# Kernel tuning notes

Hardware: AMD Instinct MI355X
Metric: run time of the kernel (lower is better)

## Reference

```python
import jax, jax.numpy as jnp
import numpy as np

N_NODES = 50000
N_EDGES = 800000
F_IN, H, C1, C2 = 256, 128, 4, 3


def gcn_conv(x, W, b, src, dst, n_nodes):
    # PyG GCNConv: add self-loops, symmetric normalization D^-1/2 A D^-1/2,
    # linear transform, scatter-add aggregation at dst, then bias.
    loop = jnp.arange(n_nodes, dtype=src.dtype)
    s = jnp.concatenate([src, loop])
    d = jnp.concatenate([dst, loop])
    deg = jax.ops.segment_sum(jnp.ones_like(d, dtype=x.dtype), d, num_segments=n_nodes)
    dinv = jnp.where(deg > 0, jax.lax.rsqrt(deg), 0.0)
    norm = dinv[s] * dinv[d]                      # [E+N]
    h = x @ W                                     # [N, out]
    msg = h[s] * norm[:, None]                    # gather + scale
    out = jax.ops.segment_sum(msg, d, num_segments=n_nodes)  # scatter-add
    return out + b


def setup_inputs() -> dict:
    key = jax.random.key(0)
    ks = jax.random.split(key, 10)
    x = jax.random.normal(ks[0], (N_NODES, F_IN), dtype=jnp.float32)
    edge_index = jax.random.randint(ks[1], (2, N_EDGES), 0, N_NODES, dtype=jnp.int32)
    def lin(k, fan_in, fan_out):
        bound = 1.0 / np.sqrt(fan_in)
        kw, kb = jax.random.split(k)
        W = jax.random.uniform(kw, (fan_in, fan_out), jnp.float32, -bound, bound)
        b = jax.random.uniform(kb, (fan_out,), jnp.float32, -bound, bound)
        return W, b
    W1, b1 = lin(ks[2], F_IN, H)
    W2, b2 = lin(ks[3], H, H)
    Wh1, bh1 = lin(ks[4], H, C1)
    Wh2, bh2 = lin(ks[5], H, C2)
    return {"x": x, "edge_index": edge_index, "W1": W1, "b1": b1,
            "W2": W2, "b2": b2, "Wh1": Wh1, "bh1": bh1, "Wh2": Wh2, "bh2": bh2}


def reference(x, edge_index, W1, b1, W2, b2, Wh1, bh1, Wh2, bh2):
    # Eval-mode forward (dropout p=0.5 is identity at inference; l2_classifier=False).
    src, dst = edge_index[0], edge_index[1]
    h = gcn_conv(x, W1, b1, src, dst, N_NODES)
    h = jax.nn.relu(h)
    h = gcn_conv(h, W2, b2, src, dst, N_NODES)
    out1 = h @ Wh1 + bh1
    out2 = h @ Wh2 + bh2
    return (out1, out2, h)
```

## Files before the change

kernel.cpp:

```cpp
#include <hip/hip_runtime.h>

#define NN 50000
#define NE 800000
#define FIN 256
#define HD 128
#define CAP 96

typedef unsigned int uint;
typedef unsigned short ushort;
typedef __attribute__((ext_vector_type(8))) short short8v;
typedef __attribute__((ext_vector_type(4))) float f32x4;

__device__ inline ushort f2bf(float f) {
    uint u = __float_as_uint(f);
    u += 0x7fffu + ((u >> 16) & 1u);
    return (ushort)(u >> 16);
}
__device__ inline void unpack2(uint u, float& a, float& b) {
    a = __uint_as_float(u << 16);
    b = __uint_as_float(u & 0xffff0000u);
}


__global__ void build_buckets(const int* __restrict__ ei, int* __restrict__ cnt,
                              int* __restrict__ bucket) {
    int e = blockIdx.x * 256 + threadIdx.x;
    if (e >= NE) return;
    int s = ei[e];
    int d = ei[NE + e];
    int pos = atomicAdd(&cnt[d], 1);
    if (pos < CAP) bucket[d * CAP + pos] = s;
}

__global__ void compute_dinv(const int* __restrict__ cnt, float* __restrict__ dinv) {
    int v = blockIdx.x * 256 + threadIdx.x;
    if (v < NN) dinv[v] = rsqrtf((float)cnt[v] + 1.0f);
}


template<int K>
__global__ void prep_wt(const float* __restrict__ W, ushort* __restrict__ Wt) {
    int idx = blockIdx.x * 256 + threadIdx.x;
    if (idx >= K * 128) return;
    int k = idx >> 7, col = idx & 127;
    Wt[col * K + k] = f2bf(W[idx]);
}


template<int K>
__global__ __launch_bounds__(256) void gemm_mfma(const float* __restrict__ A,
                                                 const ushort* __restrict__ Wt,
                                                 const float* __restrict__ dscale,
                                                 ushort* __restrict__ C, int M) {
    __shared__ ushort Ah[64][40];
    __shared__ ushort Bt[128][40];
    const int tid  = threadIdx.x;
    const int wid  = tid >> 6;
    const int lane = tid & 63;
    const int fr   = lane & 15;
    const int kg   = lane >> 4;

    const int blockRow = blockIdx.x * 64;

    f32x4 acc[8];
#pragma unroll
    for (int n = 0; n < 8; ++n) acc[n] = (f32x4){0.f, 0.f, 0.f, 0.f};

    const int s_ar = tid >> 3;
    const int s_ak = (tid & 7) << 2;

    for (int k0 = 0; k0 < K; k0 += 32) {
#pragma unroll
        for (int i = 0; i < 2; ++i) {
            int r = i * 32 + s_ar;
            int row = blockRow + r;
            float4 av = make_float4(0.f, 0.f, 0.f, 0.f);
            if (row < M) av = *(const float4*)(A + (size_t)row * K + k0 + s_ak);
            uint2 hw;
            hw.x = (uint)f2bf(av.x) | ((uint)f2bf(av.y) << 16);
            hw.y = (uint)f2bf(av.z) | ((uint)f2bf(av.w) << 16);
            *(uint2*)&Ah[r][s_ak] = hw;
        }
#pragma unroll
        for (int i = 0; i < 2; ++i) {
            int id = i * 256 + tid;
            int col = id >> 2;
            int kc = (id & 3) << 3;
            *(uint4*)&Bt[col][kc] = *(const uint4*)(Wt + (size_t)col * K + k0 + kc);
        }
        __syncthreads();
        short8v a_h = *(short8v*)&Ah[(wid << 4) + fr][kg << 3];
#pragma unroll
        for (int n = 0; n < 8; ++n) {
            short8v b = *(short8v*)&Bt[(n << 4) + fr][kg << 3];
            acc[n] = __builtin_amdgcn_mfma_f32_16x16x32_bf16(a_h, b, acc[n], 0, 0, 0);
        }
        __syncthreads();
    }

    const int rbase = blockRow + (wid << 4) + (kg << 2);
#pragma unroll
    for (int r = 0; r < 4; ++r) {
        int row = rbase + r;
        if (row < M) {
            float ds = dscale[row];
#pragma unroll
            for (int n = 0; n < 8; ++n)
                C[(size_t)row * 128 + (n << 4) + fr] = f2bf(ds * acc[n][r]);
        }
    }
}


template<int RELU, int HEADS>
__global__ __launch_bounds__(256) void aggregate(const ushort* __restrict__ hb,
                                                 const int* __restrict__ cnt,
                                                 const int* __restrict__ bucket,
                                                 const float* __restrict__ dinv,
                                                 const float* __restrict__ bias,
                                                 float* __restrict__ out,
                                                 const float* __restrict__ Wh1,
                                                 const float* __restrict__ bh1,
                                                 const float* __restrict__ Wh2,
                                                 const float* __restrict__ bh2,
                                                 float* __restrict__ out1,
                                                 float* __restrict__ out2) {
    int v = (blockIdx.x << 2) + (threadIdx.x >> 6);
    if (v >= NN) return;
    const int lane = threadIdx.x & 63;
    const int g = lane >> 4;
    const int q = lane & 15;
    int c = cnt[v]; if (c > CAP) c = CAP;
    const int total = c + 1;
    const float di = dinv[v];
    const int* bk = bucket + (size_t)v * CAP;

    float acc[8];
#pragma unroll
    for (int j = 0; j < 8; ++j) acc[j] = 0.f;

    auto slotof = [&](int k) -> int {
        return k < c ? bk[k] : (k == c ? v : NN);
    };
    auto rowload = [&](int s) -> uint4 {
        return *(const uint4*)(hb + (size_t)s * 128 + (q << 3));
    };

    int sA = slotof(g);
    int sB = slotof(4 + g);
    uint4 rA = rowload(sA);
    uint4 rB = rowload(sB);
    int sC = slotof(8 + g);
    int sD = slotof(12 + g);

    for (int e = 0; e < total; e += 8) {
        uint4 rA2 = rowload(sC);
        uint4 rB2 = rowload(sD);
        sC = slotof(e + 16 + g);
        sD = slotof(e + 20 + g);
        float f0, f1, f2, f3, f4, f5, f6, f7;
        unpack2(rA.x, f0, f1); unpack2(rA.y, f2, f3);
        unpack2(rA.z, f4, f5); unpack2(rA.w, f6, f7);
        acc[0] += f0; acc[1] += f1; acc[2] += f2; acc[3] += f3;
        acc[4] += f4; acc[5] += f5; acc[6] += f6; acc[7] += f7;
        unpack2(rB.x, f0, f1); unpack2(rB.y, f2, f3);
        unpack2(rB.z, f4, f5); unpack2(rB.w, f6, f7);
        acc[0] += f0; acc[1] += f1; acc[2] += f2; acc[3] += f3;
        acc[4] += f4; acc[5] += f5; acc[6] += f6; acc[7] += f7;
        rA = rA2; rB = rB2;
    }

#pragma unroll
    for (int j = 0; j < 8; ++j) {
        acc[j] += __shfl_xor(acc[j], 16);
        acc[j] += __shfl_xor(acc[j], 32);
    }

    float4 bb0 = *(const float4*)(bias + (q << 3));
    float4 bb1 = *(const float4*)(bias + (q << 3) + 4);
    float o[8];
    o[0] = fmaf(di, acc[0], bb0.x); o[1] = fmaf(di, acc[1], bb0.y);
    o[2] = fmaf(di, acc[2], bb0.z); o[3] = fmaf(di, acc[3], bb0.w);
    o[4] = fmaf(di, acc[4], bb1.x); o[5] = fmaf(di, acc[5], bb1.y);
    o[6] = fmaf(di, acc[6], bb1.z); o[7] = fmaf(di, acc[7], bb1.w);
    if (RELU) {
#pragma unroll
        for (int j = 0; j < 8; ++j) o[j] = fmaxf(o[j], 0.f);
    }

    if (g < 2) {
        int j0 = (g & 1) << 2;
        *(float4*)(out + (size_t)v * 128 + (q << 3) + j0) =
            make_float4(o[j0], o[j0 + 1], o[j0 + 2], o[j0 + 3]);
    }

    if (HEADS) {
        const int kb = q << 3;
        float p[7];
#pragma unroll
        for (int cc = 0; cc < 4; ++cc) {
            float s = 0.f;
#pragma unroll
            for (int j = 0; j < 8; ++j) s = fmaf(o[j], Wh1[(kb + j) * 4 + cc], s);
            p[cc] = s;
        }
#pragma unroll
        for (int cc = 0; cc < 3; ++cc) {
            float s = 0.f;
#pragma unroll
            for (int j = 0; j < 8; ++j) s = fmaf(o[j], Wh2[(kb + j) * 3 + cc], s);
            p[4 + cc] = s;
        }
#pragma unroll
        for (int i = 0; i < 7; ++i) {
            float s = p[i];
            s += __shfl_xor(s, 1);
            s += __shfl_xor(s, 2);
            s += __shfl_xor(s, 4);
            s += __shfl_xor(s, 8);
            p[i] = s;
        }
        if (lane == 0) {
            out1[(size_t)v * 4 + 0] = p[0] + bh1[0];
            out1[(size_t)v * 4 + 1] = p[1] + bh1[1];
            out1[(size_t)v * 4 + 2] = p[2] + bh1[2];
            out1[(size_t)v * 4 + 3] = p[3] + bh1[3];
            out2[(size_t)v * 3 + 0] = p[4] + bh2[0];
            out2[(size_t)v * 3 + 1] = p[5] + bh2[1];
            out2[(size_t)v * 3 + 2] = p[6] + bh2[2];
        }
    }
}


extern "C" void kernel_launch(void* const* d_in, const int* in_sizes, int n_in,
                              void* d_out, int out_size, void* d_ws, size_t ws_size,
                              hipStream_t stream) {
    const float* x   = (const float*)d_in[0];
    const int*   ei  = (const int*)d_in[1];
    const float* W1  = (const float*)d_in[2];
    const float* b1  = (const float*)d_in[3];
    const float* W2  = (const float*)d_in[4];
    const float* b2  = (const float*)d_in[5];
    const float* Wh1 = (const float*)d_in[6];
    const float* bh1 = (const float*)d_in[7];
    const float* Wh2 = (const float*)d_in[8];
    const float* bh2 = (const float*)d_in[9];

    float* out1 = (float*)d_out;
    float* out2 = out1 + (size_t)NN * 4;
    float* hout = out2 + (size_t)NN * 3;

    char* ws = (char*)d_ws;
    auto alloc = [&](size_t bytes) { char* p = ws; ws += (bytes + 255) & ~(size_t)255; return p; };
    int*    cnt    = (int*)   alloc((size_t)NN * 4);
    float*  dinv   = (float*) alloc((size_t)NN * 4);
    int*    bucket = (int*)   alloc((size_t)NN * CAP * 4);
    ushort* hlinb  = (ushort*)alloc((size_t)(NN + 1) * HD * 2);
    float*  hagg   = (float*) alloc((size_t)NN * HD * 4);
    ushort* Wt1    = (ushort*)alloc((size_t)128 * FIN * 2);
    ushort* Wt2    = (ushort*)alloc((size_t)128 * HD * 2);

    hipMemsetAsync(cnt, 0, (size_t)NN * 4, stream);
    hipMemsetAsync(hlinb + (size_t)NN * HD, 0, HD * 2, stream);
    build_buckets<<<(NE + 255) / 256, 256, 0, stream>>>(ei, cnt, bucket);
    compute_dinv<<<(NN + 255) / 256, 256, 0, stream>>>(cnt, dinv);
    prep_wt<FIN><<<(FIN * 128 + 255) / 256, 256, 0, stream>>>(W1, Wt1);
    prep_wt<HD><<<(HD * 128 + 255) / 256, 256, 0, stream>>>(W2, Wt2);

    gemm_mfma<FIN><<<(NN + 63) / 64, 256, 0, stream>>>(x, Wt1, dinv, hlinb, NN);
    aggregate<1, 0><<<(NN + 3) / 4, 256, 0, stream>>>(hlinb, cnt, bucket, dinv, b1, hagg,
                                                      nullptr, nullptr, nullptr, nullptr,
                                                      nullptr, nullptr);

    gemm_mfma<HD><<<(NN + 63) / 64, 256, 0, stream>>>(hagg, Wt2, dinv, hlinb, NN);
    aggregate<0, 1><<<(NN + 3) / 4, 256, 0, stream>>>(hlinb, cnt, bucket, dinv, b2, hout,
                                                      Wh1, bh1, Wh2, bh2, out1, out2);
}
```

Baseline: 301.7 us.

## Fuse setup kernels, store layer-1 output as bf16, retile GEMM to 32 rows

Replaces the two memsets, the weight-prep kernels and the dinv kernel with one init kernel, and computes rsqrt of the degree inline wherever it is needed. The first aggregation now writes its hidden output in bf16, so the second GEMM reads half the bytes and skips conversion. The GEMM block shrinks from 64 to 32 rows, with each wave covering 16 rows by 64 columns, which doubles the number of blocks. The change trades fewer launches and less memory traffic for less reuse of the B tile per block.

```diff
diff --git a/kernel.cpp b/kernel.cpp
--- a/kernel.cpp
+++ b/kernel.cpp
@@ -21,6 +21,16 @@
     b = __uint_as_float(u & 0xffff0000u);
 }
 
+
+__global__ void init_misc(const float* __restrict__ W1, ushort* __restrict__ Wt1,
+                          const float* __restrict__ W2, ushort* __restrict__ Wt2,
+                          int* __restrict__ cnt, ushort* __restrict__ zrow) {
+    int id = blockIdx.x * 256 + threadIdx.x;
+    if (id < NN) cnt[id] = 0;
+    if (id < FIN * 128) { int k = id >> 7, c = id & 127; Wt1[c * FIN + k] = f2bf(W1[id]); }
+    if (id < HD * 128)  { int k = id >> 7, c = id & 127; Wt2[c * HD + k]  = f2bf(W2[id]); }
+    if (id < 128) zrow[id] = 0;
+}
 
 __global__ void build_buckets(const int* __restrict__ ei, int* __restrict__ cnt,
                               int* __restrict__ bucket) {
@@ -32,54 +42,46 @@
     if (pos < CAP) bucket[d * CAP + pos] = s;
 }
 
-__global__ void compute_dinv(const int* __restrict__ cnt, float* __restrict__ dinv) {
-    int v = blockIdx.x * 256 + threadIdx.x;
-    if (v < NN) dinv[v] = rsqrtf((float)cnt[v] + 1.0f);
-}
-
-
-template<int K>
-__global__ void prep_wt(const float* __restrict__ W, ushort* __restrict__ Wt) {
-    int idx = blockIdx.x * 256 + threadIdx.x;
-    if (idx >= K * 128) return;
-    int k = idx >> 7, col = idx & 127;
-    Wt[col * K + k] = f2bf(W[idx]);
-}
-
-
-template<int K>
-__global__ __launch_bounds__(256) void gemm_mfma(const float* __restrict__ A,
+
+template<int K, int ABF>
+__global__ __launch_bounds__(256) void gemm_mfma(const void* __restrict__ Av,
                                                  const ushort* __restrict__ Wt,
-                                                 const float* __restrict__ dscale,
+                                                 const int* __restrict__ cnt,
                                                  ushort* __restrict__ C, int M) {
-    __shared__ ushort Ah[64][40];
+    __shared__ ushort Ah[32][40];
     __shared__ ushort Bt[128][40];
     const int tid  = threadIdx.x;
     const int wid  = tid >> 6;
     const int lane = tid & 63;
     const int fr   = lane & 15;
     const int kg   = lane >> 4;
-
-    const int blockRow = blockIdx.x * 64;
-
-    f32x4 acc[8];
-#pragma unroll
-    for (int n = 0; n < 8; ++n) acc[n] = (f32x4){0.f, 0.f, 0.f, 0.f};
-
-    const int s_ar = tid >> 3;
-    const int s_ak = (tid & 7) << 2;
+    const int wrow = (wid >> 1) << 4;
+    const int ncol = (wid & 1) << 6;
+
+    const int blockRow = blockIdx.x * 32;
+
+    f32x4 acc[4];
+#pragma unroll
+    for (int n = 0; n < 4; ++n) acc[n] = (f32x4){0.f, 0.f, 0.f, 0.f};
+
+    const int s_r  = tid >> 3;
+    const int s_k  = (tid & 7) << 2;
+    const int s_row = blockRow + s_r;
 
     for (int k0 = 0; k0 < K; k0 += 32) {
-#pragma unroll
-        for (int i = 0; i < 2; ++i) {
-            int r = i * 32 + s_ar;
-            int row = blockRow + r;
-            float4 av = make_float4(0.f, 0.f, 0.f, 0.f);
-            if (row < M) av = *(const float4*)(A + (size_t)row * K + k0 + s_ak);
+        if (ABF) {
+            const ushort* A = (const ushort*)Av;
+            uint2 v = make_uint2(0u, 0u);
+            if (s_row < M) v = *(const uint2*)(A + (size_t)s_row * K + k0 + s_k);
+            *(uint2*)&Ah[s_r][s_k] = v;
+        } else {
+            const float* A = (const float*)Av;
+            float4 v = make_float4(0.f, 0.f, 0.f, 0.f);
+            if (s_row < M) v = *(const float4*)(A + (size_t)s_row * K + k0 + s_k);
             uint2 hw;
-            hw.x = (uint)f2bf(av.x) | ((uint)f2bf(av.y) << 16);
-            hw.y = (uint)f2bf(av.z) | ((uint)f2bf(av.w) << 16);
-            *(uint2*)&Ah[r][s_ak] = hw;
+            hw.x = (uint)f2bf(v.x) | ((uint)f2bf(v.y) << 16);
+            hw.y = (uint)f2bf(v.z) | ((uint)f2bf(v.w) << 16);
+            *(uint2*)&Ah[s_r][s_k] = hw;
         }
 #pragma unroll
         for (int i = 0; i < 2; ++i) {
@@ -89,36 +91,36 @@
             *(uint4*)&Bt[col][kc] = *(const uint4*)(Wt + (size_t)col * K + k0 + kc);
         }
         __syncthreads();
-        short8v a_h = *(short8v*)&Ah[(wid << 4) + fr][kg << 3];
-#pragma unroll
-        for (int n = 0; n < 8; ++n) {
-            short8v b = *(short8v*)&Bt[(n << 4) + fr][kg << 3];
-            acc[n] = __builtin_amdgcn_mfma_f32_16x16x32_bf16(a_h, b, acc[n], 0, 0, 0);
+        short8v a = *(short8v*)&Ah[wrow + fr][kg << 3];
+#pragma unroll
+        for (int n = 0; n < 4; ++n) {
+            short8v b = *(short8v*)&Bt[ncol + (n << 4) + fr][kg << 3];
+            acc[n] = __builtin_amdgcn_mfma_f32_16x16x32_bf16(a, b, acc[n], 0, 0, 0);
         }
         __syncthreads();
     }
 
-    const int rbase = blockRow + (wid << 4) + (kg << 2);
+    const int rbase = blockRow + wrow + (kg << 2);
 #pragma unroll
     for (int r = 0; r < 4; ++r) {
         int row = rbase + r;
         if (row < M) {
-            float ds = dscale[row];
-#pragma unroll
-            for (int n = 0; n < 8; ++n)
-                C[(size_t)row * 128 + (n << 4) + fr] = f2bf(ds * acc[n][r]);
-        }
-    }
-}
-
-
-template<int RELU, int HEADS>
+            float ds = rsqrtf((float)cnt[row] + 1.0f);
+#pragma unroll
+            for (int n = 0; n < 4; ++n)
+                C[(size_t)row * 128 + ncol + (n << 4) + fr] = f2bf(ds * acc[n][r]);
+        }
+    }
+}
+
+
+template<int RELU, int HEADS, int OBF>
 __global__ __launch_bounds__(256) void aggregate(const ushort* __restrict__ hb,
                                                  const int* __restrict__ cnt,
                                                  const int* __restrict__ bucket,
-                                                 const float* __restrict__ dinv,
                                                  const float* __restrict__ bias,
-                                                 float* __restrict__ out,
+                                                 float* __restrict__ outf,
+                                                 ushort* __restrict__ outb,
                                                  const float* __restrict__ Wh1,
                                                  const float* __restrict__ bh1,
                                                  const float* __restrict__ Wh2,
@@ -130,9 +132,10 @@
     const int lane = threadIdx.x & 63;
     const int g = lane >> 4;
     const int q = lane & 15;
-    int c = cnt[v]; if (c > CAP) c = CAP;
+    const int craw = cnt[v];
+    const int c = craw < CAP ? craw : CAP;
     const int total = c + 1;
-    const float di = dinv[v];
+    const float di = rsqrtf((float)craw + 1.0f);
     const int* bk = bucket + (size_t)v * CAP;
 
     float acc[8];
@@ -188,10 +191,21 @@
         for (int j = 0; j < 8; ++j) o[j] = fmaxf(o[j], 0.f);
     }
 
-    if (g < 2) {
-        int j0 = (g & 1) << 2;
-        *(float4*)(out + (size_t)v * 128 + (q << 3) + j0) =
-            make_float4(o[j0], o[j0 + 1], o[j0 + 2], o[j0 + 3]);
+    if (OBF) {
+        if (g == 0) {
+            uint4 w;
+            w.x = (uint)f2bf(o[0]) | ((uint)f2bf(o[1]) << 16);
+            w.y = (uint)f2bf(o[2]) | ((uint)f2bf(o[3]) << 16);
+            w.z = (uint)f2bf(o[4]) | ((uint)f2bf(o[5]) << 16);
+            w.w = (uint)f2bf(o[6]) | ((uint)f2bf(o[7]) << 16);
+            *(uint4*)(outb + (size_t)v * 128 + (q << 3)) = w;
+        }
+    } else {
+        if (g < 2) {
+            int j0 = (g & 1) << 2;
+            *(float4*)(outf + (size_t)v * 128 + (q << 3) + j0) =
+                make_float4(o[j0], o[j0 + 1], o[j0 + 2], o[j0 + 3]);
+        }
     }
 
     if (HEADS) {
@@ -254,26 +268,24 @@
     char* ws = (char*)d_ws;
     auto alloc = [&](size_t bytes) { char* p = ws; ws += (bytes + 255) & ~(size_t)255; return p; };
     int*    cnt    = (int*)   alloc((size_t)NN * 4);
-    float*  dinv   = (float*) alloc((size_t)NN * 4);
     int*    bucket = (int*)   alloc((size_t)NN * CAP * 4);
     ushort* hlinb  = (ushort*)alloc((size_t)(NN + 1) * HD * 2);
-    float*  hagg   = (float*) alloc((size_t)NN * HD * 4);
+    ushort* haggb  = (ushort*)alloc((size_t)NN * HD * 2);
     ushort* Wt1    = (ushort*)alloc((size_t)128 * FIN * 2);
     ushort* Wt2    = (ushort*)alloc((size_t)128 * HD * 2);
 
-    hipMemsetAsync(cnt, 0, (size_t)NN * 4, stream);
-    hipMemsetAsync(hlinb + (size_t)NN * HD, 0, HD * 2, stream);
+    init_misc<<<(NN + 255) / 256, 256, 0, stream>>>(W1, Wt1, W2, Wt2, cnt,
+                                                    hlinb + (size_t)NN * HD);
     build_buckets<<<(NE + 255) / 256, 256, 0, stream>>>(ei, cnt, bucket);
-    compute_dinv<<<(NN + 255) / 256, 256, 0, stream>>>(cnt, dinv);
-    prep_wt<FIN><<<(FIN * 128 + 255) / 256, 256, 0, stream>>>(W1, Wt1);
-    prep_wt<HD><<<(HD * 128 + 255) / 256, 256, 0, stream>>>(W2, Wt2);
-
-    gemm_mfma<FIN><<<(NN + 63) / 64, 256, 0, stream>>>(x, Wt1, dinv, hlinb, NN);
-    aggregate<1, 0><<<(NN + 3) / 4, 256, 0, stream>>>(hlinb, cnt, bucket, dinv, b1, hagg,
-                                                      nullptr, nullptr, nullptr, nullptr,
-                                                      nullptr, nullptr);
-
-    gemm_mfma<HD><<<(NN + 63) / 64, 256, 0, stream>>>(hagg, Wt2, dinv, hlinb, NN);
-    aggregate<0, 1><<<(NN + 3) / 4, 256, 0, stream>>>(hlinb, cnt, bucket, dinv, b2, hout,
-                                                      Wh1, bh1, Wh2, bh2, out1, out2);
-}
+
+    gemm_mfma<FIN, 0><<<(NN + 31) / 32, 256, 0, stream>>>(x, Wt1, cnt, hlinb, NN);
+    aggregate<1, 0, 1><<<(NN + 3) / 4, 256, 0, stream>>>(hlinb, cnt, bucket, b1,
+                                                         nullptr, haggb,
+                                                         nullptr, nullptr, nullptr, nullptr,
+                                                         nullptr, nullptr);
+
+    gemm_mfma<HD, 1><<<(NN + 31) / 32, 256, 0, stream>>>(haggb, Wt2, cnt, hlinb, NN);
+    aggregate<0, 1, 0><<<(NN + 3) / 4, 256, 0, stream>>>(hlinb, cnt, bucket, b2,
+                                                         hout, nullptr,
+                                                         Wh1, bh1, Wh2, bh2, out1, out2);
+}
```

New measurement: 286.0 us. -5.2%, faster.
